# Performance work log

Hardware: AMD Instinct MI355X
Metric: run time of the kernel (lower is better)

The kernel has to match this reference:

```python
import jax, jax.numpy as jnp
import numpy as np

DIM = 1024
HEADS = 16
HEAD_DIM = DIM // HEADS
MLP_HID = 4 * DIM
EPS = 1e-5


def layer_norm(x, g, b):
    mu = jnp.mean(x, axis=-1, keepdims=True)
    var = jnp.mean(jnp.square(x - mu), axis=-1, keepdims=True)
    return (x - mu) * jax.lax.rsqrt(var + EPS) * g + b


def setup_inputs() -> dict:
    key = jax.random.key(0)
    ks = jax.random.split(key, 8)
    s_in = 1.0 / np.sqrt(DIM)
    s_hid = 1.0 / np.sqrt(MLP_HID)
    return {
        "x": jax.random.normal(ks[0], (4, 2048, DIM), dtype=jnp.float32),
        "qkv_w": jax.random.uniform(ks[1], (3 * DIM, DIM), jnp.float32, -s_in, s_in),
        "proj_w": jax.random.uniform(ks[2], (DIM, DIM), jnp.float32, -s_in, s_in),
        "proj_b": jnp.zeros((DIM,), jnp.float32),
        "ln1_g": jnp.ones((DIM,), jnp.float32),
        "ln1_b": jnp.zeros((DIM,), jnp.float32),
        "w1": jax.random.uniform(ks[3], (MLP_HID, DIM), jnp.float32, -s_in, s_in),
        "b1": jnp.zeros((MLP_HID,), jnp.float32),
        "prelu_a": jnp.asarray(0.25, jnp.float32),
        "w2": jax.random.uniform(ks[4], (DIM, MLP_HID), jnp.float32, -s_hid, s_hid),
        "b2": jnp.zeros((DIM,), jnp.float32),
        "ln2_g": jnp.ones((DIM,), jnp.float32),
        "ln2_b": jnp.zeros((DIM,), jnp.float32),
    }


def reference(x, qkv_w, proj_w, proj_b, ln1_g, ln1_b, w1, b1, prelu_a, w2, b2, ln2_g, ln2_b):
    B, N, C = x.shape
    scale = HEAD_DIM ** (-0.5)

    # Multi-head self-attention (full NxN scores, softmax over keys)
    qkv = (x @ qkv_w.T).reshape(B, N, 3, HEADS, HEAD_DIM)
    qkv = jnp.transpose(qkv, (2, 0, 3, 1, 4))  # [3, B, H, N, hd]
    q, k, v = qkv[0] * scale, qkv[1], qkv[2]
    attn = jax.nn.softmax(jnp.einsum("bhnd,bhmd->bhnm", q, k), axis=-1)
    o = jnp.einsum("bhnm,bhmd->bhnd", attn, v)
    o = jnp.transpose(o, (0, 2, 1, 3)).reshape(B, N, C)
    o = o @ proj_w.T + proj_b

    # Post-norm residual 1
    x = layer_norm(x + o, ln1_g, ln1_b)

    # MLP: Linear -> (Dropout=identity in eval) -> PReLU -> Linear
    h = x @ w1.T + b1
    h = jnp.where(h >= 0, h, prelu_a * h)
    h = h @ w2.T + b2

    # Post-norm residual 2
    return layer_norm(x + h, ln2_g, ln2_b)
```

## Files before the change

### kernel.cpp

```cpp
#include <hip/hip_runtime.h>


typedef __attribute__((ext_vector_type(8))) short short8;
typedef __attribute__((ext_vector_type(4))) short short4v;
typedef __attribute__((ext_vector_type(4))) float floatx4;
typedef __attribute__((ext_vector_type(4))) int int4v;

__device__ __forceinline__ float bf2f(unsigned short u) {
    return __uint_as_float(((unsigned int)u) << 16);
}
__device__ __forceinline__ unsigned short f2bf(float f) {
    unsigned int u = __float_as_uint(f);
    u += 0x7FFFu + ((u >> 16) & 1u);
    return (unsigned short)(u >> 16);
}
__device__ __forceinline__ int pack2bf(float a, float b) {
    return (int)f2bf(a) | ((int)f2bf(b) << 16);
}
__device__ __forceinline__ unsigned int cvt_pk_bf16(float lo, float hi) {
    unsigned int r;
    asm("v_cvt_pk_bf16_f32 %0, %1, %2" : "=v"(r) : "v"(lo), "v"(hi));
    return r;
}

#define Q_PRESCALE 0.18033688011112043f

#if __has_builtin(__builtin_amdgcn_exp2f)
__device__ __forceinline__ float fast_exp2(float x) { return __builtin_amdgcn_exp2f(x); }
#else
__device__ __forceinline__ float fast_exp2(float x) { return __expf(x * 0.6931471805599453f); }
#endif

#if __has_builtin(__builtin_amdgcn_permlane32_swap) && __has_builtin(__builtin_amdgcn_permlane16_swap)
#define HAVE_PERMLANE 1
#else
#define HAVE_PERMLANE 0
#endif

__device__ __forceinline__ void async16(const unsigned short* g, unsigned short* l) {
    __builtin_amdgcn_global_load_lds(
        (const __attribute__((address_space(1))) unsigned int*)g,
        (__attribute__((address_space(3))) unsigned int*)l, 16, 0, 0);
}

#define BARRIER() do { __builtin_amdgcn_s_barrier(); asm volatile("" ::: "memory"); } while (0)
#define VMCNT(n)  asm volatile("s_waitcnt vmcnt(" #n ")" ::: "memory")

__global__ __launch_bounds__(256)
void cvt_f2b(const float* __restrict__ in, unsigned short* __restrict__ out) {
    const int i = (blockIdx.x * 256 + threadIdx.x) * 4;
    float4 v = *(const float4*)&in[i];
    short4v o;
    o[0] = (short)f2bf(v.x); o[1] = (short)f2bf(v.y);
    o[2] = (short)f2bf(v.z); o[3] = (short)f2bf(v.w);
    *(short4v*)&out[i] = o;
}

__global__ __launch_bounds__(512, 2)
void gemm256(const unsigned short* __restrict__ A,
             const unsigned short* __restrict__ W,
             const float* __restrict__ bias,
             const float* __restrict__ prelu,
             unsigned short* __restrict__ C,
             int N, int K, int qcols, int NNT) {
    __shared__ alignas(16) unsigned short lA[2][256 * 64];
    __shared__ alignas(16) unsigned short lB[2][256 * 64];

    const int nwg = gridDim.x;
    const int orig = blockIdx.x;
    const int q8 = nwg >> 3, r8 = nwg & 7, xx = orig & 7, rest = orig >> 3;
    const int wgid = (xx < r8 ? xx * (q8 + 1) : r8 * (q8 + 1) + (xx - r8) * q8) + rest;
    const int mt = wgid / NNT, nt = wgid % NNT;
    const int m0 = mt * 256, n0 = nt * 256;

    const int tid  = threadIdx.x;
    const int lane = tid & 63;
    const int wave = tid >> 6;
    const int lr = lane & 15, lq = lane >> 4;
    const int wrow = (wave >> 2) * 64;
    const int wcol = (wave & 3) * 32;
    const int srow = lane >> 3;
    const int scol = ((lane & 7) ^ srow) << 3;
    const int kx = lr & 7;

    const int NT = K >> 6;

    floatx4 acc[2][2][4][2] = {};
    short8 af[4][2], b0[2][2], b1[2][2];

    auto stA = [&](int d, int tt, int h) {
        #pragma unroll
        for (int it = 0; it < 2; ++it) {
            const int rb = h * 128 + (wave * 2 + it) * 8;
            async16(&A[(size_t)(m0 + rb + srow) * K + tt * 64 + scol], &lA[d][rb * 64]);
        }
    };
    auto stB = [&](int d, int tt, int h) {
        #pragma unroll
        for (int it = 0; it < 2; ++it) {
            const int rb = h * 128 + (wave * 2 + it) * 8;
            async16(&W[(size_t)(n0 + rb + srow) * K + tt * 64 + scol], &lB[d][rb * 64]);
        }
    };

#define RD_AF(dd, half)                                                        \
    _Pragma("unroll") for (int i = 0; i < 4; ++i)                              \
    _Pragma("unroll") for (int s = 0; s < 2; ++s)                              \
        af[i][s] = *(const short8*)&lA[dd][((half) * 128 + wrow + i * 16 + lr) * 64 + \
                                           (((s * 4 + lq) ^ kx) << 3)]
#define RD_B0(dd)                                                              \
    _Pragma("unroll") for (int j = 0; j < 2; ++j)                              \
    _Pragma("unroll") for (int s = 0; s < 2; ++s)                              \
        b0[j][s] = *(const short8*)&lB[dd][(wcol + j * 16 + lr) * 64 +         \
                                           (((s * 4 + lq) ^ kx) << 3)]
#define RD_B1(dd)                                                              \
    _Pragma("unroll") for (int j = 0; j < 2; ++j)                              \
    _Pragma("unroll") for (int s = 0; s < 2; ++s)                              \
        b1[j][s] = *(const short8*)&lB[dd][(128 + wcol + j * 16 + lr) * 64 +   \
                                           (((s * 4 + lq) ^ kx) << 3)]
#define MM256(mh, nh, BB)                                                      \
    _Pragma("unroll") for (int s = 0; s < 2; ++s)                              \
    _Pragma("unroll") for (int i = 0; i < 4; ++i)                              \
    _Pragma("unroll") for (int j = 0; j < 2; ++j)                              \
        acc[mh][nh][i][j] = __builtin_amdgcn_mfma_f32_16x16x32_bf16(           \
            af[i][s], BB[j][s], acc[mh][nh][i][j], 0, 0, 0)

    stA(0, 0, 0); stB(0, 0, 0); stB(0, 0, 1); stA(0, 0, 1);
    stA(1, 1, 0); stB(1, 1, 0); stB(1, 1, 1);
    VMCNT(6);
    BARRIER();
    RD_AF(0, 0);
    RD_B0(0);

    for (int t = 0; t < NT; ++t) {
        const int d = t & 1, e = d ^ 1;

        RD_B1(d);
        if (t + 1 < NT) stA(e, t + 1, 1);
        BARRIER();
        __builtin_amdgcn_s_setprio(1);
        MM256(0, 0, b0);
        __builtin_amdgcn_s_setprio(0);
        BARRIER();

        if (t + 2 < NT) stA(d, t + 2, 0);
        BARRIER();
        __builtin_amdgcn_s_setprio(1);
        MM256(0, 1, b1);
        __builtin_amdgcn_s_setprio(0);
        RD_AF(d, 1);
        BARRIER();

        if (t + 2 < NT) stB(d, t + 2, 0);
        BARRIER();
        __builtin_amdgcn_s_setprio(1);
        MM256(1, 1, b1);
        __builtin_amdgcn_s_setprio(0);
        if (t + 2 < NT)      { VMCNT(4); }
        else if (t + 1 < NT) { VMCNT(0); }
        BARRIER();

        if (t + 2 < NT) stB(d, t + 2, 1);
        BARRIER();
        __builtin_amdgcn_s_setprio(1);
        MM256(1, 0, b0);
        __builtin_amdgcn_s_setprio(0);
        if (t + 1 < NT) {
            RD_AF(e, 0);
            RD_B0(e);
        }
        BARRIER();
    }

#undef RD_AF
#undef RD_B0
#undef RD_B1
#undef MM256

    const bool hasb = (bias != nullptr);
    const bool hasp = (prelu != nullptr);
    const float slope = hasp ? prelu[0] : 0.f;
    #pragma unroll
    for (int mh = 0; mh < 2; ++mh)
        #pragma unroll
        for (int nh = 0; nh < 2; ++nh)
            #pragma unroll
            for (int j = 0; j < 2; ++j) {
                const int gc = n0 + nh * 128 + wcol + j * 16 + lr;
                const float bv = hasb ? bias[gc] : 0.f;
                const float cs = (gc < qcols) ? Q_PRESCALE : 1.f;
                #pragma unroll
                for (int i = 0; i < 4; ++i) {
                    const int gr = m0 + mh * 128 + wrow + i * 16 + lq * 4;
                    #pragma unroll
                    for (int r = 0; r < 4; ++r) {
                        float v = acc[mh][nh][i][j][r] + bv;
                        if (hasp && v < 0.f) v *= slope;
                        C[(size_t)(gr + r) * N + gc] = f2bf(v * cs);
                    }
                }
            }
}

__global__ __launch_bounds__(512, 2)
void gemm128(const unsigned short* __restrict__ A,
             const unsigned short* __restrict__ W,
             const float* __restrict__ bias,
             const float* __restrict__ prelu,
             unsigned short* __restrict__ C,
             int N, int K, int qcols, int NNT) {
    __shared__ alignas(16) unsigned short lA[2][128 * 64];
    __shared__ alignas(16) unsigned short lB[2][256 * 64];

    const int nwg = gridDim.x;
    const int orig = blockIdx.x;
    const int q8 = nwg >> 3, r8 = nwg & 7, xx = orig & 7, rest = orig >> 3;
    const int wgid = (xx < r8 ? xx * (q8 + 1) : r8 * (q8 + 1) + (xx - r8) * q8) + rest;
    const int mt = wgid / NNT, nt = wgid % NNT;
    const int m0 = mt * 128, n0 = nt * 256;

    const int tid  = threadIdx.x;
    const int lane = tid & 63;
    const int wave = tid >> 6;
    const int lr = lane & 15, lq = lane >> 4;
    const int wrow = (wave >> 2) * 64;
    const int wcol = (wave & 3) * 32;
    const int srow = lane >> 3;
    const int scol = ((lane & 7) ^ srow) << 3;
    const int kx = lr & 7;

    const int NT = K >> 6;

    floatx4 acc[2][4][2] = {};
    short8 af[4][2], b0[2][2], b1[2][2];

    auto stA = [&](int d, int tt) {
        #pragma unroll
        for (int it = 0; it < 2; ++it) {
            const int rb = (wave * 2 + it) * 8;
            async16(&A[(size_t)(m0 + rb + srow) * K + tt * 64 + scol], &lA[d][rb * 64]);
        }
    };
    auto stB = [&](int d, int tt, int h) {
        #pragma unroll
        for (int it = 0; it < 2; ++it) {
            const int rb = (wave * 2 + it) * 8;
            async16(&W[(size_t)(n0 + h * 128 + rb + srow) * K + tt * 64 + scol],
                    &lB[d][(h * 128 + rb) * 64]);
        }
    };

#define RD_AF(dd)                                                              \
    _Pragma("unroll") for (int i = 0; i < 4; ++i)                              \
    _Pragma("unroll") for (int s = 0; s < 2; ++s)                              \
        af[i][s] = *(const short8*)&lA[dd][(wrow + i * 16 + lr) * 64 +         \
                                           (((s * 4 + lq) ^ kx) << 3)]
#define RD_B0(dd)                                                              \
    _Pragma("unroll") for (int j = 0; j < 2; ++j)                              \
    _Pragma("unroll") for (int s = 0; s < 2; ++s)                              \
        b0[j][s] = *(const short8*)&lB[dd][(wcol + j * 16 + lr) * 64 +         \
                                           (((s * 4 + lq) ^ kx) << 3)]
#define RD_B1(dd)                                                              \
    _Pragma("unroll") for (int j = 0; j < 2; ++j)                              \
    _Pragma("unroll") for (int s = 0; s < 2; ++s)                              \
        b1[j][s] = *(const short8*)&lB[dd][(128 + wcol + j * 16 + lr) * 64 +   \
                                           (((s * 4 + lq) ^ kx) << 3)]
#define MM128(nh, BB)                                                          \
    _Pragma("unroll") for (int s = 0; s < 2; ++s)                              \
    _Pragma("unroll") for (int i = 0; i < 4; ++i)                              \
    _Pragma("unroll") for (int j = 0; j < 2; ++j)                              \
        acc[nh][i][j] = __builtin_amdgcn_mfma_f32_16x16x32_bf16(               \
            af[i][s], BB[j][s], acc[nh][i][j], 0, 0, 0)

    stA(0, 0); stB(0, 0, 0); stB(0, 0, 1);
    stA(1, 1); stB(1, 1, 0);
    VMCNT(4);
    BARRIER();
    RD_AF(0);
    RD_B0(0);

    for (int t = 0; t < NT; ++t) {
        const int d = t & 1, e = d ^ 1;

        RD_B1(d);
        if (t + 1 < NT) stB(e, t + 1, 1);
        BARRIER();
        __builtin_amdgcn_s_setprio(1);
        MM128(0, b0);
        __builtin_amdgcn_s_setprio(0);
        if (t + 1 < NT) { VMCNT(2); }
        BARRIER();

        if (t + 2 < NT) { stA(d, t + 2); stB(d, t + 2, 0); }
        BARRIER();
        __builtin_amdgcn_s_setprio(1);
        MM128(1, b1);
        __builtin_amdgcn_s_setprio(0);
        if (t + 2 < NT)      { VMCNT(4); }
        else if (t + 1 < NT) { VMCNT(0); }
        if (t + 1 < NT) {
            RD_AF(e);
            RD_B0(e);
        }
        BARRIER();
    }

#undef RD_AF
#undef RD_B0
#undef RD_B1
#undef MM128

    const bool hasb = (bias != nullptr);
    const bool hasp = (prelu != nullptr);
    const float slope = hasp ? prelu[0] : 0.f;
    #pragma unroll
    for (int nh = 0; nh < 2; ++nh)
        #pragma unroll
        for (int j = 0; j < 2; ++j) {
            const int gc = n0 + nh * 128 + wcol + j * 16 + lr;
            const float bv = hasb ? bias[gc] : 0.f;
            const float cs = (gc < qcols) ? Q_PRESCALE : 1.f;
            #pragma unroll
            for (int i = 0; i < 4; ++i) {
                const int gr = m0 + wrow + i * 16 + lq * 4;
                #pragma unroll
                for (int r = 0; r < 4; ++r) {
                    float v = acc[nh][i][j][r] + bv;
                    if (hasp && v < 0.f) v *= slope;
                    C[(size_t)(gr + r) * N + gc] = f2bf(v * cs);
                }
            }
        }
}

__global__ __launch_bounds__(256)
void transpose_v(const unsigned short* __restrict__ qkv,
                 unsigned short* __restrict__ vt) {
    const int kt = blockIdx.x;
    const int bh = blockIdx.y;
    const int b = bh >> 4, h = bh & 15;
    __shared__ unsigned short tile[64 * 65];
    for (int t = threadIdx.x; t < 512; t += 256) {
        const int key = t >> 3, c8 = (t & 7) << 3;
        short8 v8 = *(const short8*)&qkv[((size_t)(b * 2048 + kt * 64 + key)) * 3072 +
                                         2048 + h * 64 + c8];
        #pragma unroll
        for (int e = 0; e < 8; ++e)
            tile[key * 65 + c8 + e] = (unsigned short)v8[e];
    }
    __syncthreads();
    for (int t = threadIdx.x; t < 512; t += 256) {
        const int d = t >> 3, k8 = (t & 7) << 3;
        short8 o;
        #pragma unroll
        for (int e = 0; e < 8; ++e)
            o[e] = (short)tile[(k8 + e) * 65 + d];
        *(short8*)&vt[((size_t)bh * 64 + d) * 2048 + kt * 64 + k8] = o;
    }
}

__global__ __launch_bounds__(256, 2)
void attn_kernel(const unsigned short* __restrict__ qkv,
                 const unsigned short* __restrict__ vt,
                 unsigned short* __restrict__ o_attn) {
    const int id = blockIdx.x;
    const int qg = id >> 6;
    const int bh = id & 63;
    const int b = bh >> 4, h = bh & 15;
    const int tid  = threadIdx.x;
    const int lane = tid & 63;
    const int wave = tid >> 6;
    const int lr = lane & 15;
    const int lq = lane >> 4;
    const int q0 = (qg * 4 + wave) * 64;
    const size_t row0 = (size_t)(b * 2048) * 3072;

    __shared__ alignas(16) unsigned short lK[2][64 * 64];
    __shared__ alignas(16) unsigned short lV[2][64 * 64];

    short8 qf[4][2];
    #pragma unroll
    for (int j = 0; j < 4; ++j)
        #pragma unroll
        for (int s = 0; s < 2; ++s)
            qf[j][s] = *(const short8*)&qkv[row0 + (size_t)(q0 + j * 16 + lr) * 3072 +
                                            h * 64 + s * 32 + lq * 8];

    floatx4 oacc[4][4] = {};
    float l_i[4] = {0.f, 0.f, 0.f, 0.f};

    const int srow = lane >> 3;
    const int scol = (((lane & 7) ^ srow)) << 3;
    const int kx = lr & 7;

    auto stage = [&](int bi, int kc) {
        #pragma unroll
        for (int it2 = 0; it2 < 2; ++it2) {
            const int it = wave * 2 + it2;
            const int row = it * 8 + srow;
            async16(&qkv[row0 + (size_t)(kc + row) * 3072 + 1024 + h * 64 + scol],
                    &lK[bi][it * 512 + lane * 8]);
            async16(&vt[((size_t)bh * 64 + row) * 2048 + kc + scol],
                    &lV[bi][it * 512 + lane * 8]);
        }
    };

    asm volatile("s_waitcnt vmcnt(0)" ::: "memory");
    stage(0, 0);

    #pragma unroll 1
    for (int c = 0; c < 32; ++c) {
        const int cur = c & 1;
        if (c + 1 < 32) {
            stage(cur ^ 1, (c + 1) * 64);
            asm volatile("s_waitcnt vmcnt(4)" ::: "memory");
        } else {
            asm volatile("s_waitcnt vmcnt(0)" ::: "memory");
        }
        __builtin_amdgcn_s_barrier();
        asm volatile("" ::: "memory");

        floatx4 sacc[4][4] = {};
        #pragma unroll
        for (int s = 0; s < 2; ++s) {
            short8 kf[4];
            #pragma unroll
            for (int i = 0; i < 4; ++i) {
                const int r = i * 16 + lr;
                kf[i] = *(const short8*)&lK[cur][r * 64 + (((s * 4 + lq) ^ kx) << 3)];
            }
            #pragma unroll
            for (int i = 0; i < 4; ++i)
                #pragma unroll
                for (int j = 0; j < 4; ++j)
                    sacc[i][j] = __builtin_amdgcn_mfma_f32_16x16x32_bf16(
                        kf[i], qf[j][s], sacc[i][j], 0, 0, 0);
        }

        unsigned int pkd[4][4][2];
        #pragma unroll
        for (int i = 0; i < 4; ++i)
            #pragma unroll
            for (int j = 0; j < 4; ++j) {
                const float e0 = fast_exp2(sacc[i][j][0]);
                const float e1 = fast_exp2(sacc[i][j][1]);
                const float e2 = fast_exp2(sacc[i][j][2]);
                const float e3 = fast_exp2(sacc[i][j][3]);
                l_i[j] += (e0 + e1) + (e2 + e3);
                pkd[i][j][0] = cvt_pk_bf16(e0, e1);
                pkd[i][j][1] = cvt_pk_bf16(e2, e3);
            }

        #pragma unroll
        for (int s = 0; s < 2; ++s) {
            short8 vf[4];
            #pragma unroll
            for (int i = 0; i < 4; ++i) {
                const int r = i * 16 + lr;
                vf[i] = *(const short8*)&lV[cur][r * 64 + (((s * 4 + lq) ^ kx) << 3)];
            }
            short8 bq[4];
            #pragma unroll
            for (int j = 0; j < 4; ++j) {
                int4v iv;
#if HAVE_PERMLANE
                auto p0 = __builtin_amdgcn_permlane32_swap(
                    pkd[2 * s][j][0], pkd[2 * s + 1][j][0], false, false);
                auto w0 = __builtin_amdgcn_permlane16_swap(p0[0], p0[1], false, false);
                auto p1 = __builtin_amdgcn_permlane32_swap(
                    pkd[2 * s][j][1], pkd[2 * s + 1][j][1], false, false);
                auto w1 = __builtin_amdgcn_permlane16_swap(p1[0], p1[1], false, false);
                iv[0] = (int)w0[0]; iv[1] = (int)w1[0];
                iv[2] = (int)w0[1]; iv[3] = (int)w1[1];
#else
                const int src0 = lr + ((lq & 1) * 2) * 16;
                const int src1 = src0 + 16;
                const bool hi = (lq >> 1) != 0;
                int a0 = __shfl((int)pkd[2 * s][j][0], src0, 64);
                int c0 = __shfl((int)pkd[2 * s + 1][j][0], src0, 64);
                int a1 = __shfl((int)pkd[2 * s][j][1], src0, 64);
                int c1 = __shfl((int)pkd[2 * s + 1][j][1], src0, 64);
                int a2 = __shfl((int)pkd[2 * s][j][0], src1, 64);
                int c2 = __shfl((int)pkd[2 * s + 1][j][0], src1, 64);
                int a3 = __shfl((int)pkd[2 * s][j][1], src1, 64);
                int c3 = __shfl((int)pkd[2 * s + 1][j][1], src1, 64);
                iv[0] = hi ? c0 : a0;
                iv[1] = hi ? c1 : a1;
                iv[2] = hi ? c2 : a2;
                iv[3] = hi ? c3 : a3;
#endif
                bq[j] = __builtin_bit_cast(short8, iv);
            }
            #pragma unroll
            for (int j = 0; j < 4; ++j)
                #pragma unroll
                for (int i = 0; i < 4; ++i)
                    oacc[i][j] = __builtin_amdgcn_mfma_f32_16x16x32_bf16(
                        vf[i], bq[j], oacc[i][j], 0, 0, 0);
        }

        asm volatile("s_waitcnt lgkmcnt(0)" ::: "memory");
        __builtin_amdgcn_s_barrier();
        asm volatile("" ::: "memory");
    }

    #pragma unroll
    for (int j = 0; j < 4; ++j) {
        l_i[j] += __shfl_xor(l_i[j], 16, 64);
        l_i[j] += __shfl_xor(l_i[j], 32, 64);
        const float rl = 1.f / l_i[j];
        const int q = q0 + j * 16 + lr;
        #pragma unroll
        for (int i = 0; i < 4; ++i) {
            int2 pk;
            pk.x = pack2bf(oacc[i][j][0] * rl, oacc[i][j][1] * rl);
            pk.y = pack2bf(oacc[i][j][2] * rl, oacc[i][j][3] * rl);
            *(int2*)&o_attn[((size_t)(b * 2048 + q)) * 1024 + h * 64 + i * 16 + lq * 4] = pk;
        }
    }
}

__global__ __launch_bounds__(256)
void ln_f32_bf16(const float* __restrict__ x,
                 const unsigned short* __restrict__ res,
                 const float* __restrict__ g,
                 const float* __restrict__ bta,
                 unsigned short* __restrict__ out) {
    const int row = blockIdx.x;
    const int t = threadIdx.x;
    const size_t base = (size_t)row * 1024;

    float4 xv = *(const float4*)&x[base + t * 4];
    short4v rv = *(const short4v*)&res[base + t * 4];
    float v[4] = { xv.x + bf2f((unsigned short)rv[0]),
                   xv.y + bf2f((unsigned short)rv[1]),
                   xv.z + bf2f((unsigned short)rv[2]),
                   xv.w + bf2f((unsigned short)rv[3]) };
    float s = 0.f, s2 = 0.f;
    #pragma unroll
    for (int k = 0; k < 4; ++k) { s += v[k]; s2 += v[k] * v[k]; }
    #pragma unroll
    for (int off = 32; off > 0; off >>= 1) {
        s  += __shfl_xor(s, off, 64);
        s2 += __shfl_xor(s2, off, 64);
    }
    __shared__ float red[8];
    const int wave = t >> 6;
    if ((t & 63) == 0) { red[wave] = s; red[4 + wave] = s2; }
    __syncthreads();
    s  = red[0] + red[1] + red[2] + red[3];
    s2 = red[4] + red[5] + red[6] + red[7];
    const float mean = s * (1.f / 1024.f);
    const float var  = fmaxf(s2 * (1.f / 1024.f) - mean * mean, 0.f);
    const float inv  = rsqrtf(var + 1e-5f);

    short4v ov;
    #pragma unroll
    for (int k = 0; k < 4; ++k) {
        int c = t * 4 + k;
        ov[k] = (short)f2bf((v[k] - mean) * inv * g[c] + bta[c]);
    }
    *(short4v*)&out[base + t * 4] = ov;
}

__global__ __launch_bounds__(256)
void ln_bf16_f32(const unsigned short* __restrict__ x,
                 const unsigned short* __restrict__ res,
                 const float* __restrict__ g,
                 const float* __restrict__ bta,
                 float* __restrict__ out) {
    const int row = blockIdx.x;
    const int t = threadIdx.x;
    const size_t base = (size_t)row * 1024;

    short4v xv = *(const short4v*)&x[base + t * 4];
    short4v rv = *(const short4v*)&res[base + t * 4];
    float v[4];
    float s = 0.f, s2 = 0.f;
    #pragma unroll
    for (int k = 0; k < 4; ++k) {
        v[k] = bf2f((unsigned short)xv[k]) + bf2f((unsigned short)rv[k]);
        s += v[k];
        s2 += v[k] * v[k];
    }
    #pragma unroll
    for (int off = 32; off > 0; off >>= 1) {
        s  += __shfl_xor(s, off, 64);
        s2 += __shfl_xor(s2, off, 64);
    }
    __shared__ float red[8];
    const int wave = t >> 6;
    if ((t & 63) == 0) { red[wave] = s; red[4 + wave] = s2; }
    __syncthreads();
    s  = red[0] + red[1] + red[2] + red[3];
    s2 = red[4] + red[5] + red[6] + red[7];
    const float mean = s * (1.f / 1024.f);
    const float var  = fmaxf(s2 * (1.f / 1024.f) - mean * mean, 0.f);
    const float inv  = rsqrtf(var + 1e-5f);

    float4 ov;
    ov.x = (v[0] - mean) * inv * g[t * 4 + 0] + bta[t * 4 + 0];
    ov.y = (v[1] - mean) * inv * g[t * 4 + 1] + bta[t * 4 + 1];
    ov.z = (v[2] - mean) * inv * g[t * 4 + 2] + bta[t * 4 + 2];
    ov.w = (v[3] - mean) * inv * g[t * 4 + 3] + bta[t * 4 + 3];
    *(float4*)&out[base + t * 4] = ov;
}

extern "C" void kernel_launch(void* const* d_in, const int* in_sizes, int n_in,
                              void* d_out, int out_size, void* d_ws, size_t ws_size,
                              hipStream_t stream) {
    const float* x      = (const float*)d_in[0];
    const float* qkv_w  = (const float*)d_in[1];
    const float* proj_w = (const float*)d_in[2];
    const float* proj_b = (const float*)d_in[3];
    const float* ln1_g  = (const float*)d_in[4];
    const float* ln1_b  = (const float*)d_in[5];
    const float* w1     = (const float*)d_in[6];
    const float* b1     = (const float*)d_in[7];
    const float* prelu  = (const float*)d_in[8];
    const float* w2     = (const float*)d_in[9];
    const float* b2     = (const float*)d_in[10];
    const float* ln2_g  = (const float*)d_in[11];
    const float* ln2_b  = (const float*)d_in[12];
    float* out = (float*)d_out;

    char* ws = (char*)d_ws;
    const size_t MB = 1024 * 1024;
    unsigned short* wqkvb  = (unsigned short*)(ws);
    unsigned short* wprojb = (unsigned short*)(ws + 6 * MB);
    unsigned short* w1b    = (unsigned short*)(ws + 8 * MB);
    unsigned short* w2b    = (unsigned short*)(ws + 16 * MB);
    unsigned short* xb     = (unsigned short*)(ws + 24 * MB);
    unsigned short* vtb    = (unsigned short*)(ws + 24 * MB);
    unsigned short* qkvb   = (unsigned short*)(ws + 40 * MB);
    unsigned short* oat    = (unsigned short*)(ws + 88 * MB);
    unsigned short* pout   = (unsigned short*)(ws + 24 * MB);
    unsigned short* x1b    = (unsigned short*)(ws + 40 * MB);
    unsigned short* h1     = (unsigned short*)(ws + 56 * MB);
    unsigned short* h2     = (unsigned short*)(ws + 24 * MB);

    cvt_f2b<<<8192, 256, 0, stream>>>(x,      xb);
    cvt_f2b<<<3072, 256, 0, stream>>>(qkv_w,  wqkvb);
    cvt_f2b<<<1024, 256, 0, stream>>>(proj_w, wprojb);
    cvt_f2b<<<4096, 256, 0, stream>>>(w1,     w1b);
    cvt_f2b<<<4096, 256, 0, stream>>>(w2,     w2b);

    gemm128<<<dim3(64 * 12), 512, 0, stream>>>(xb, wqkvb, nullptr, nullptr,
                                               qkvb, 3072, 1024, 1024, 12);
    transpose_v<<<dim3(32, 64), 256, 0, stream>>>(qkvb, vtb);
    attn_kernel<<<512, 256, 0, stream>>>(qkvb, vtb, oat);
    gemm128<<<dim3(64 * 4), 512, 0, stream>>>(oat, wprojb, proj_b, nullptr,
                                              pout, 1024, 1024, 0, 4);
    ln_f32_bf16<<<8192, 256, 0, stream>>>(x, pout, ln1_g, ln1_b, x1b);
    gemm256<<<dim3(32 * 16), 512, 0, stream>>>(x1b, w1b, b1, prelu,
                                               h1, 4096, 1024, 0, 16);
    gemm128<<<dim3(64 * 4), 512, 0, stream>>>(h1, w2b, b2, nullptr,
                                              h2, 1024, 4096, 0, 4);
    ln_bf16_f32<<<8192, 256, 0, stream>>>(x1b, h2, ln2_g, ln2_b, out);
}
```

Before: 506.0 us.

## Switch GEMM kernels to 32x32x16 bf16 MFMA tiles

Both the 256 and 128 GEMM kernels now use 32x32x16 MFMA instructions with 16-wide float accumulators instead of 16x16x32, with LDS fragment addressing and the epilogue row mapping reworked to match. Larger MFMA tiles need fewer LDS fragment reads per FLOP and fewer instructions. In gemm128 the LDS read schedule also changes: A and B0 fragments are loaded at the start of each iteration rather than prefetched at the end of the previous one, with explicit lgkmcnt waits. That gives up LDS-read/compute overlap in exchange for simpler register pressure.

```diff
diff --git a/kernel.cpp b/kernel.cpp
--- a/kernel.cpp
+++ b/kernel.cpp
@@ -4,6 +4,7 @@
 typedef __attribute__((ext_vector_type(8))) short short8;
 typedef __attribute__((ext_vector_type(4))) short short4v;
 typedef __attribute__((ext_vector_type(4))) float floatx4;
+typedef __attribute__((ext_vector_type(16))) float floatx16;
 typedef __attribute__((ext_vector_type(4))) int int4v;
 
 __device__ __forceinline__ float bf2f(unsigned short u) {
@@ -45,6 +46,7 @@
 
 #define BARRIER() do { __builtin_amdgcn_s_barrier(); asm volatile("" ::: "memory"); } while (0)
 #define VMCNT(n)  asm volatile("s_waitcnt vmcnt(" #n ")" ::: "memory")
+#define LGKM0()   asm volatile("s_waitcnt lgkmcnt(0)" ::: "memory")
 
 __global__ __launch_bounds__(256)
 void cvt_f2b(const float* __restrict__ in, unsigned short* __restrict__ out) {
@@ -76,17 +78,17 @@
     const int tid  = threadIdx.x;
     const int lane = tid & 63;
     const int wave = tid >> 6;
-    const int lr = lane & 15, lq = lane >> 4;
+    const int l31 = lane & 31, kg = lane >> 5;
+    const int kx = l31 & 7;
     const int wrow = (wave >> 2) * 64;
     const int wcol = (wave & 3) * 32;
     const int srow = lane >> 3;
     const int scol = ((lane & 7) ^ srow) << 3;
-    const int kx = lr & 7;
 
     const int NT = K >> 6;
 
-    floatx4 acc[2][2][4][2] = {};
-    short8 af[4][2], b0[2][2], b1[2][2];
+    floatx16 acc[2][2][2] = {};
+    short8 af[2][4], b0[4], b1[4];
 
     auto stA = [&](int d, int tt, int h) {
         #pragma unroll
@@ -104,26 +106,23 @@
     };
 
 #define RD_AF(dd, half)                                                        \
-    _Pragma("unroll") for (int i = 0; i < 4; ++i)                              \
-    _Pragma("unroll") for (int s = 0; s < 2; ++s)                              \
-        af[i][s] = *(const short8*)&lA[dd][((half) * 128 + wrow + i * 16 + lr) * 64 + \
-                                           (((s * 4 + lq) ^ kx) << 3)]
+    _Pragma("unroll") for (int mf = 0; mf < 2; ++mf)                           \
+    _Pragma("unroll") for (int ks = 0; ks < 4; ++ks)                           \
+        af[mf][ks] = *(const short8*)&lA[dd][((half) * 128 + wrow + mf * 32 + l31) * 64 + \
+                                             (((ks * 2 + kg) ^ kx) << 3)]
 #define RD_B0(dd)                                                              \
-    _Pragma("unroll") for (int j = 0; j < 2; ++j)                              \
-    _Pragma("unroll") for (int s = 0; s < 2; ++s)                              \
-        b0[j][s] = *(const short8*)&lB[dd][(wcol + j * 16 + lr) * 64 +         \
-                                           (((s * 4 + lq) ^ kx) << 3)]
+    _Pragma("unroll") for (int ks = 0; ks < 4; ++ks)                           \
+        b0[ks] = *(const short8*)&lB[dd][(wcol + l31) * 64 +                   \
+                                         (((ks * 2 + kg) ^ kx) << 3)]
 #define RD_B1(dd)                                                              \
-    _Pragma("unroll") for (int j = 0; j < 2; ++j)                              \
-    _Pragma("unroll") for (int s = 0; s < 2; ++s)                              \
-        b1[j][s] = *(const short8*)&lB[dd][(128 + wcol + j * 16 + lr) * 64 +   \
-                                           (((s * 4 + lq) ^ kx) << 3)]
+    _Pragma("unroll") for (int ks = 0; ks < 4; ++ks)                           \
+        b1[ks] = *(const short8*)&lB[dd][(128 + wcol + l31) * 64 +             \
+                                         (((ks * 2 + kg) ^ kx) << 3)]
 #define MM256(mh, nh, BB)                                                      \
-    _Pragma("unroll") for (int s = 0; s < 2; ++s)                              \
-    _Pragma("unroll") for (int i = 0; i < 4; ++i)                              \
-    _Pragma("unroll") for (int j = 0; j < 2; ++j)                              \
-        acc[mh][nh][i][j] = __builtin_amdgcn_mfma_f32_16x16x32_bf16(           \
-            af[i][s], BB[j][s], acc[mh][nh][i][j], 0, 0, 0)
+    _Pragma("unroll") for (int ks = 0; ks < 4; ++ks)                           \
+    _Pragma("unroll") for (int mf = 0; mf < 2; ++mf)                           \
+        acc[mh][nh][mf] = __builtin_amdgcn_mfma_f32_32x32x16_bf16(             \
+            af[mf][ks], BB[ks], acc[mh][nh][mf], 0, 0, 0)
 
     stA(0, 0, 0); stB(0, 0, 0); stB(0, 0, 1); stA(0, 0, 1);
     stA(1, 1, 0); stB(1, 1, 0); stB(1, 1, 1);
@@ -183,23 +182,22 @@
     #pragma unroll
     for (int mh = 0; mh < 2; ++mh)
         #pragma unroll
-        for (int nh = 0; nh < 2; ++nh)
-            #pragma unroll
-            for (int j = 0; j < 2; ++j) {
-                const int gc = n0 + nh * 128 + wcol + j * 16 + lr;
-                const float bv = hasb ? bias[gc] : 0.f;
-                const float cs = (gc < qcols) ? Q_PRESCALE : 1.f;
+        for (int nh = 0; nh < 2; ++nh) {
+            const int gc = n0 + nh * 128 + wcol + l31;
+            const float bv = hasb ? bias[gc] : 0.f;
+            const float cs = (gc < qcols) ? Q_PRESCALE : 1.f;
+            #pragma unroll
+            for (int mf = 0; mf < 2; ++mf) {
+                const int grb = m0 + mh * 128 + wrow + mf * 32 + 4 * kg;
                 #pragma unroll
-                for (int i = 0; i < 4; ++i) {
-                    const int gr = m0 + mh * 128 + wrow + i * 16 + lq * 4;
-                    #pragma unroll
-                    for (int r = 0; r < 4; ++r) {
-                        float v = acc[mh][nh][i][j][r] + bv;
-                        if (hasp && v < 0.f) v *= slope;
-                        C[(size_t)(gr + r) * N + gc] = f2bf(v * cs);
-                    }
+                for (int r = 0; r < 16; ++r) {
+                    const int gr = grb + (r & 3) + 8 * (r >> 2);
+                    float v = acc[mh][nh][mf][r] + bv;
+                    if (hasp && v < 0.f) v *= slope;
+                    C[(size_t)gr * N + gc] = f2bf(v * cs);
                 }
             }
+        }
 }
 
 __global__ __launch_bounds__(512, 2)
@@ -222,17 +220,17 @@
     const int tid  = threadIdx.x;
     const int lane = tid & 63;
     const int wave = tid >> 6;
-    const int lr = lane & 15, lq = lane >> 4;
+    const int l31 = lane & 31, kg = lane >> 5;
+    const int kx = l31 & 7;
     const int wrow = (wave >> 2) * 64;
     const int wcol = (wave & 3) * 32;
     const int srow = lane >> 3;
     const int scol = ((lane & 7) ^ srow) << 3;
-    const int kx = lr & 7;
 
     const int NT = K >> 6;
 
-    floatx4 acc[2][4][2] = {};
-    short8 af[4][2], b0[2][2], b1[2][2];
+    floatx16 acc[2][2] = {};
+    short8 af[2][4], b0[4], b1[4];
 
     auto stA = [&](int d, int tt) {
         #pragma unroll
@@ -251,57 +249,51 @@
     };
 
 #define RD_AF(dd)                                                              \
-    _Pragma("unroll") for (int i = 0; i < 4; ++i)                              \
-    _Pragma("unroll") for (int s = 0; s < 2; ++s)                              \
-        af[i][s] = *(const short8*)&lA[dd][(wrow + i * 16 + lr) * 64 +         \
-                                           (((s * 4 + lq) ^ kx) << 3)]
+    _Pragma("unroll") for (int mf = 0; mf < 2; ++mf)                           \
+    _Pragma("unroll") for (int ks = 0; ks < 4; ++ks)                           \
+        af[mf][ks] = *(const short8*)&lA[dd][(wrow + mf * 32 + l31) * 64 +     \
+                                             (((ks * 2 + kg) ^ kx) << 3)]
 #define RD_B0(dd)                                                              \
-    _Pragma("unroll") for (int j = 0; j < 2; ++j)                              \
-    _Pragma("unroll") for (int s = 0; s < 2; ++s)                              \
-        b0[j][s] = *(const short8*)&lB[dd][(wcol + j * 16 + lr) * 64 +         \
-                                           (((s * 4 + lq) ^ kx) << 3)]
+    _Pragma("unroll") for (int ks = 0; ks < 4; ++ks)                           \
+        b0[ks] = *(const short8*)&lB[dd][(wcol + l31) * 64 +                   \
+                                         (((ks * 2 + kg) ^ kx) << 3)]
 #define RD_B1(dd)                                                              \
-    _Pragma("unroll") for (int j = 0; j < 2; ++j)                              \
-    _Pragma("unroll") for (int s = 0; s < 2; ++s)                              \
-        b1[j][s] = *(const short8*)&lB[dd][(128 + wcol + j * 16 + lr) * 64 +   \
-                                           (((s * 4 + lq) ^ kx) << 3)]
+    _Pragma("unroll") for (int ks = 0; ks < 4; ++ks)                           \
+        b1[ks] = *(const short8*)&lB[dd][(128 + wcol + l31) * 64 +             \
+                                         (((ks * 2 + kg) ^ kx) << 3)]
 #define MM128(nh, BB)                                                          \
-    _Pragma("unroll") for (int s = 0; s < 2; ++s)                              \
-    _Pragma("unroll") for (int i = 0; i < 4; ++i)                              \
-    _Pragma("unroll") for (int j = 0; j < 2; ++j)                              \
-        acc[nh][i][j] = __builtin_amdgcn_mfma_f32_16x16x32_bf16(               \
-            af[i][s], BB[j][s], acc[nh][i][j], 0, 0, 0)
+    _Pragma("unroll") for (int ks = 0; ks < 4; ++ks)                           \
+    _Pragma("unroll") for (int mf = 0; mf < 2; ++mf)                           \
+        acc[nh][mf] = __builtin_amdgcn_mfma_f32_32x32x16_bf16(                 \
+            af[mf][ks], BB[ks], acc[nh][mf], 0, 0, 0)
 
     stA(0, 0); stB(0, 0, 0); stB(0, 0, 1);
     stA(1, 1); stB(1, 1, 0);
     VMCNT(4);
     BARRIER();
-    RD_AF(0);
-    RD_B0(0);
 
     for (int t = 0; t < NT; ++t) {
         const int d = t & 1, e = d ^ 1;
 
-        RD_B1(d);
+        RD_AF(d);
+        RD_B0(d);
         if (t + 1 < NT) stB(e, t + 1, 1);
         BARRIER();
+        LGKM0();
         __builtin_amdgcn_s_setprio(1);
         MM128(0, b0);
         __builtin_amdgcn_s_setprio(0);
-        if (t + 1 < NT) { VMCNT(2); }
-        BARRIER();
-
+        BARRIER();
+
+        RD_B1(d);
         if (t + 2 < NT) { stA(d, t + 2); stB(d, t + 2, 0); }
         BARRIER();
+        LGKM0();
         __builtin_amdgcn_s_setprio(1);
         MM128(1, b1);
         __builtin_amdgcn_s_setprio(0);
         if (t + 2 < NT)      { VMCNT(4); }
         else if (t + 1 < NT) { VMCNT(0); }
-        if (t + 1 < NT) {
-            RD_AF(e);
-            RD_B0(e);
-        }
         BARRIER();
     }
 
@@ -314,23 +306,22 @@
     const bool hasp = (prelu != nullptr);
     const float slope = hasp ? prelu[0] : 0.f;
     #pragma unroll
-    for (int nh = 0; nh < 2; ++nh)
-        #pragma unroll
-        for (int j = 0; j < 2; ++j) {
-            const int gc = n0 + nh * 128 + wcol + j * 16 + lr;
-            const float bv = hasb ? bias[gc] : 0.f;
-            const float cs = (gc < qcols) ? Q_PRESCALE : 1.f;
-            #pragma unroll
-            for (int i = 0; i < 4; ++i) {
-                const int gr = m0 + wrow + i * 16 + lq * 4;
-                #pragma unroll
-                for (int r = 0; r < 4; ++r) {
-                    float v = acc[nh][i][j][r] + bv;
-                    if (hasp && v < 0.f) v *= slope;
-                    C[(size_t)(gr + r) * N + gc] = f2bf(v * cs);
-                }
+    for (int nh = 0; nh < 2; ++nh) {
+        const int gc = n0 + nh * 128 + wcol + l31;
+        const float bv = hasb ? bias[gc] : 0.f;
+        const float cs = (gc < qcols) ? Q_PRESCALE : 1.f;
+        #pragma unroll
+        for (int mf = 0; mf < 2; ++mf) {
+            const int grb = m0 + wrow + mf * 32 + 4 * kg;
+            #pragma unroll
+            for (int r = 0; r < 16; ++r) {
+                const int gr = grb + (r & 3) + 8 * (r >> 2);
+                float v = acc[nh][mf][r] + bv;
+                if (hasp && v < 0.f) v *= slope;
+                C[(size_t)gr * N + gc] = f2bf(v * cs);
             }
         }
+    }
 }
 
 __global__ __launch_bounds__(256)
```

Result: slower. 525.4 us (+3.8%).
